# Performance work log

Hardware: AMD Instinct MI355X
Metric: run time of the kernel (lower is better)

The kernel has to match this reference:

```python
import jax, jax.numpy as jnp
import numpy as np

BETA = 0.25  # loss_beta


def setup_inputs() -> dict:
    key = jax.random.key(0)
    k1, k2 = jax.random.split(key)
    data = jax.random.normal(k1, (65536, 256), dtype=jnp.float32)       # [N, D]
    codebooks = jax.random.normal(k2, (4, 1024, 256), dtype=jnp.float32)  # [L, K, D]
    return {"data": data, "codebooks": codebooks}


def _quantize_level(r, cb):
    # r: [N, D], cb: [K, D]
    # L2 distances via ||r||^2 + ||c||^2 - 2 r @ c^T (matches torch.addmm form)
    d2 = ((r * r).sum(-1, keepdims=True)
          + (cb * cb).sum(-1)[None, :]
          - 2.0 * (r @ cb.T))                      # [N, K]
    ids = jnp.argmin(d2, axis=-1)                  # [N]
    q = cb[ids]                                    # nearest-code gather, [N, D]
    return q, ids


def reference(data, codebooks):
    sg = jax.lax.stop_gradient
    r = data
    z_q = jnp.zeros_like(data)
    loss = jnp.zeros((), dtype=data.dtype)
    zq_list, id_list = [], []
    for i in range(codebooks.shape[0]):  # small fixed number of codebook levels
        r_in = r
        q, ids = _quantize_level(r_in, codebooks[i])
        q_st = r_in + sg(q - r_in)                 # straight-through estimator
        z_q = z_q + q_st
        # commitment + codebook loss (standard RQ-VAE)
        loss = loss + BETA * jnp.mean((sg(q) - r_in) ** 2) \
                    + jnp.mean((q - sg(r_in)) ** 2)
        r = r_in - q                               # residual for next level
        zq_list.append(z_q)
        id_list.append(ids)
    zq_stack = jnp.stack(zq_list)                  # [L, N, D] accumulated quantizations
    semantic_ids = jnp.stack(id_list, axis=-1)     # [N, L]
    return zq_stack, semantic_ids, loss
```

## Files before the change

kernel.cpp:

```cpp
#include <hip/hip_runtime.h>
#include <hip/hip_bf16.h>


#define NROWS   65536
#define DIM     256
#define KCODES  1024
#define LEVELS  4
#define CH      (NROWS * DIM)
#define IDS_OFF (LEVELS * CH)

#define BM      256
#define NCHUNK  8
#define CAP     32
#define MARGIN  8.0f
#define CHUNK_USH 32768
#define LVL_USH 262144

typedef __attribute__((ext_vector_type(8))) short bf16x8;
typedef __attribute__((ext_vector_type(4))) float f32x4;
typedef const __attribute__((address_space(1))) void* gp_t;
typedef __attribute__((address_space(3))) void* lp_t;

__device__ __forceinline__ unsigned short f2bf(float x) {
    __hip_bfloat16 h = __float2bfloat16(x);
    unsigned short r; __builtin_memcpy(&r, &h, 2); return r;
}
__device__ __forceinline__ float bf2f(unsigned short u) {
    __hip_bfloat16 h; __builtin_memcpy(&h, &u, 2); return __bfloat162float(h);
}

__global__ __launch_bounds__(64) void k_prep(const float* __restrict__ cb,
                                             unsigned short* __restrict__ cbw,
                                             float* __restrict__ cn2w,
                                             double* __restrict__ cn2d) {
    int cr = blockIdx.x;
    int L = cr >> 10, c = cr & 1023;
    int l = threadIdx.x;
    float4 v = *(const float4*)(cb + (size_t)cr * DIM + l * 4);
    ushort4 st;
    st.x = f2bf(v.x); st.y = f2bf(v.y); st.z = f2bf(v.z); st.w = f2bf(v.w);
    int b = l * 8;
    int kk = b >> 6, g = (b >> 4) & 3, h = (b & 15) >> 1;
    int idx = ((((L * 16 + (c >> 6)) * 4 + ((c >> 4) & 3)) * 8 + kk) * 64
               + (g * 16 + (c & 15))) * 8 + h;
    *(ushort4*)(cbw + idx) = st;
    float f0 = bf2f(st.x), f1 = bf2f(st.y), f2 = bf2f(st.z), f3 = bf2f(st.w);
    float sq = f0 * f0 + f1 * f1 + f2 * f2 + f3 * f3;
    double dq = (double)v.x * v.x + (double)v.y * v.y
              + (double)v.z * v.z + (double)v.w * v.w;
    #pragma unroll
    for (int m = 32; m; m >>= 1) {
        sq += __shfl_xor(sq, m);
        dq += __shfl_xor(dq, m);
    }
    if (l == 0) { cn2w[cr] = sq; cn2d[cr] = dq; }
}

__global__ __launch_bounds__(1024) void k_score(
    const float* rsrc,
    const float* __restrict__ cbf,
    const unsigned short* __restrict__ cbwL,
    const float* __restrict__ cn2L,
    const double* __restrict__ cn2dL,
    int* __restrict__ wid_out,
    float* rnext,
    int level)
{
    __shared__ unsigned short cbuf[2 * CHUNK_USH];
    __shared__ unsigned short cand[BM * CAP];
    __shared__ int cnt[BM];
    __shared__ int winid[BM];

    const int tid = threadIdx.x;
    const int w = tid >> 6, l = tid & 63;
    const int g = l >> 4, li = l & 15;
    const int rows0 = blockIdx.x * BM;

    #define STAGE(T) do {                                                      \
        const unsigned short* _g = cbwL + (T) * CHUNK_USH;                     \
        unsigned short* _d = &cbuf[((T) & 1) * CHUNK_USH];                     \
        _Pragma("unroll")                                                      \
        for (int _r = 0; _r < 4; ++_r)                                         \
            __builtin_amdgcn_global_load_lds((gp_t)(_g + _r * 8192 + tid * 8), \
                                             (lp_t)(_d + _r * 8192 + tid * 8), \
                                             16, 0, 0);                        \
    } while (0)

    STAGE(0);
    if (tid < BM) cnt[tid] = 0;

    bf16x8 af[8];
    {
        int row = rows0 + w * 16 + li;
        const float* rp = rsrc + (size_t)row * DIM;
        #pragma unroll
        for (int kk = 0; kk < 8; ++kk) {
            int d0 = kk * 32 + 8 * g;
            float4 v0 = *(const float4*)(rp + d0);
            float4 v1 = *(const float4*)(rp + d0 + 4);
            bf16x8 t;
            t[0] = (short)f2bf(v0.x); t[1] = (short)f2bf(v0.y);
            t[2] = (short)f2bf(v0.z); t[3] = (short)f2bf(v0.w);
            t[4] = (short)f2bf(v1.x); t[5] = (short)f2bf(v1.y);
            t[6] = (short)f2bf(v1.z); t[7] = (short)f2bf(v1.w);
            af[kk] = t;
        }
    }

    float minv[4];
    float sbuf[8][4];
    #pragma unroll
    for (int rg = 0; rg < 4; ++rg) minv[rg] = 3.0e38f;

    __syncthreads();

    for (int kc = 0; kc < NCHUNK; ++kc) {
        if (kc < NCHUNK - 1) STAGE(kc + 1);
        const unsigned short* fb = &cbuf[(kc & 1) * CHUNK_USH];

        #pragma unroll
        for (int nt = 0; nt < 8; ++nt) {
            f32x4 acc = {0.f, 0.f, 0.f, 0.f};
            const unsigned short* fp8 = fb + (nt * 8) * 512 + l * 8;
            #pragma unroll
            for (int kk = 0; kk < 8; ++kk) {
                bf16x8 bfr = *(const bf16x8*)(fp8 + kk * 512);
                acc = __builtin_amdgcn_mfma_f32_16x16x32_bf16(af[kk], bfr, acc, 0, 0, 0);
            }
            float c2 = cn2L[kc * 128 + nt * 16 + li];
            #pragma unroll
            for (int rg = 0; rg < 4; ++rg) {
                float v = __builtin_fmaf(-2.f, acc[rg], c2);
                sbuf[nt][rg] = v;
                minv[rg] = fminf(minv[rg], v);
            }
        }

        float rowm[4];
        #pragma unroll
        for (int rg = 0; rg < 4; ++rg) {
            float v = minv[rg];
            v = fminf(v, __shfl_xor(v, 1));
            v = fminf(v, __shfl_xor(v, 2));
            v = fminf(v, __shfl_xor(v, 4));
            v = fminf(v, __shfl_xor(v, 8));
            minv[rg] = v;
            rowm[rg] = v + MARGIN;
        }

        #pragma unroll
        for (int nt = 0; nt < 8; ++nt) {
            bool any = false;
            #pragma unroll
            for (int rg = 0; rg < 4; ++rg)
                any |= (sbuf[nt][rg] < rowm[rg]);
            if (__any(any)) {
                #pragma unroll
                for (int rg = 0; rg < 4; ++rg)
                    if (sbuf[nt][rg] < rowm[rg]) {
                        int row = w * 16 + 4 * g + rg;
                        int slot = atomicAdd(&cnt[row], 1);
                        if (slot < CAP)
                            cand[row * CAP + slot] =
                                (unsigned short)(kc * 128 + nt * 16 + li);
                    }
            }
        }
        __syncthreads();
    }

    {
        const int gg = l >> 4;
        const int q4 = l & 15;
        for (int rr = 0; rr < 16; ++rr) {
            int row = w * 16 + rr;
            int k = cnt[row];
            if (k == 1) {
                if (l == 0) winid[row] = (int)cand[row * CAP];
                continue;
            }
            bool list = (k >= 1 && k <= CAP);
            int total = list ? k : KCODES;
            int grow = rows0 + row;
            const float* rrow = rsrc + (size_t)grow * DIM;
            float4 rv[4];
            #pragma unroll
            for (int j = 0; j < 4; ++j)
                rv[j] = *(const float4*)(rrow + q4 * 4 + j * 64);
            double bestS = 1.0e300; int bestI = 0x7fffffff;
            for (int base = 0; base < total; base += 4) {
                int slot = base + gg;
                bool valid = slot < total;
                int code = valid ? (list ? (int)cand[row * CAP + slot] : slot) : 0;
                const float* crow = cbf + (size_t)code * DIM;
                double acc = 0.0;
                #pragma unroll
                for (int j = 0; j < 4; ++j) {
                    float4 cv = *(const float4*)(crow + q4 * 4 + j * 64);
                    acc = fma((double)cv.x, (double)rv[j].x, acc);
                    acc = fma((double)cv.y, (double)rv[j].y, acc);
                    acc = fma((double)cv.z, (double)rv[j].z, acc);
                    acc = fma((double)cv.w, (double)rv[j].w, acc);
                }
                #pragma unroll
                for (int m = 1; m <= 8; m <<= 1) acc += __shfl_xor(acc, m);
                double s = valid ? (cn2dL[code] - 2.0 * acc) : 1.0e300;
                #pragma unroll
                for (int gq = 0; gq < 4; ++gq) {
                    double sg = __shfl(s, gq * 16);
                    int cg = __shfl(code, gq * 16);
                    if ((base + gq) < total &&
                        (sg < bestS || (sg == bestS && cg < bestI))) {
                        bestS = sg; bestI = cg;
                    }
                }
            }
            if (l == 0) winid[row] = bestI;
        }
    }
    __syncthreads();

    if (tid < BM)
        wid_out[(size_t)(rows0 + tid) * LEVELS + level] = winid[tid];
    if (rnext) {
        #pragma unroll
        for (int it = 0; it < 16; ++it) {
            int rowloc = it * 16 + w;
            int grow = rows0 + rowloc;
            int d0 = l * 4;
            int code = winid[rowloc];
            float4 q = *(const float4*)(cbf + (size_t)code * DIM + d0);
            float4 r = *(const float4*)(rsrc + (size_t)grow * DIM + d0);
            float4 rn;
            rn.x = r.x - q.x; rn.y = r.y - q.y;
            rn.z = r.z - q.z; rn.w = r.w - q.w;
            *(float4*)(rnext + (size_t)grow * DIM + d0) = rn;
        }
    }
}

__global__ __launch_bounds__(256) void k_final(
    const float* __restrict__ data,
    const float* __restrict__ cbf0,
    int* wid,
    float* __restrict__ zq,
    double* __restrict__ blockpart)
{
    __shared__ float wl[4];
    const int tid = threadIdx.x;
    const int w = tid >> 6, l = tid & 63;
    const int rows0 = blockIdx.x * 32;
    float lacc = 0.f;
    #pragma unroll
    for (int i = 0; i < 8; ++i) {
        int grow = rows0 + i * 4 + w;
        int4 c4 = *(const int4*)(wid + (size_t)grow * LEVELS);
        int d0 = l * 4;
        float4 r = *(const float4*)(data + (size_t)grow * DIM + d0);
        float4 z = {0.f, 0.f, 0.f, 0.f};
        int codes[4] = {c4.x, c4.y, c4.z, c4.w};
        #pragma unroll
        for (int lv = 0; lv < LEVELS; ++lv) {
            const float* crow = cbf0 + ((size_t)lv * KCODES + codes[lv]) * DIM;
            float4 q = *(const float4*)(crow + d0);
            float dx = q.x - r.x, dy = q.y - r.y, dz = q.z - r.z, dw = q.w - r.w;
            z.x += (r.x + dx); z.y += (r.y + dy);
            z.z += (r.z + dz); z.w += (r.w + dw);
            *(float4*)(zq + (size_t)lv * CH + (size_t)grow * DIM + d0) = z;
            lacc += dx * dx + dy * dy + dz * dz + dw * dw;
            r.x = -dx; r.y = -dy; r.z = -dz; r.w = -dw;
        }
        if (l == 0) {
            float4 f; f.x = (float)codes[0]; f.y = (float)codes[1];
            f.z = (float)codes[2]; f.w = (float)codes[3];
            *(float4*)((float*)wid + (size_t)grow * LEVELS) = f;
        }
    }
    #pragma unroll
    for (int m = 32; m; m >>= 1) lacc += __shfl_xor(lacc, m);
    if (l == 0) wl[w] = lacc;
    __syncthreads();
    if (tid == 0)
        blockpart[blockIdx.x] =
            (double)wl[0] + (double)wl[1] + (double)wl[2] + (double)wl[3];
}

__global__ __launch_bounds__(256) void k_loss(const double* __restrict__ part,
                                              float* __restrict__ loss) {
    __shared__ double sd[256];
    int tid = threadIdx.x;
    double a = 0.0;
    #pragma unroll
    for (int i = 0; i < 8; ++i) a += part[i * 256 + tid];
    sd[tid] = a; __syncthreads();
    for (int s = 128; s > 0; s >>= 1) {
        if (tid < s) sd[tid] += sd[tid + s];
        __syncthreads();
    }
    if (tid == 0) *loss = (float)(sd[0] * (1.25 / 16777216.0));
}

extern "C" void kernel_launch(void* const* d_in, const int* in_sizes, int n_in,
                              void* d_out, int out_size, void* d_ws, size_t ws_size,
                              hipStream_t stream) {
    const float* data = (const float*)d_in[0];
    const float* cb   = (const float*)d_in[1];
    float* out  = (float*)d_out;
    float* zq   = out;
    int*   wid  = (int*)(out + IDS_OFF);
    float* loss = out + IDS_OFF + NROWS * LEVELS;
    char* ws = (char*)d_ws;
    unsigned short* cbw = (unsigned short*)ws;
    float*  cn2w  = (float*)(ws + (size_t)LEVELS * LVL_USH * 2);
    double* cn2d  = (double*)(ws + (size_t)LEVELS * LVL_USH * 2 + 16384);
    double* bpart = (double*)(ws + (size_t)LEVELS * LVL_USH * 2 + 16384 + 32768);
    float* rscr = zq + (size_t)3 * CH;

    k_prep<<<LEVELS * KCODES, 64, 0, stream>>>(cb, cbw, cn2w, cn2d);
    for (int lv = 0; lv < LEVELS; ++lv) {
        const float* rsrc = (lv == 0) ? data : rscr;
        float* rnext = (lv < 3) ? rscr : nullptr;
        k_score<<<NROWS / BM, 1024, 0, stream>>>(
            rsrc, cb + (size_t)lv * KCODES * DIM, cbw + (size_t)lv * LVL_USH,
            cn2w + (size_t)lv * KCODES, cn2d + (size_t)lv * KCODES,
            wid, rnext, lv);
    }
    k_final<<<NROWS / 32, 256, 0, stream>>>(data, cb, wid, zq, bpart);
    k_loss<<<1, 256, 0, stream>>>(bpart, loss);
}
```

Baseline: 482.0 us.

## Fuse four per-level scoring launches into one persistent kernel with cross-level prefetch

Merges the four per-level k_score launches into a single k_score4 kernel in which each block loops over all codebook levels for its own 256 rows. This is possible because the residual rows a block needs are the ones it wrote itself. The first chunk of the next level's codebook is prefetched into LDS while the current level's refinement runs, which removes launch gaps and tail drain between levels. Each level still re-reads the residual through global memory, which is now reached through __restrict__ pointers with only a block-level fence. That aliasing and the write-then-read ordering carry some correctness risk.

```diff
diff --git a/kernel.cpp b/kernel.cpp
--- a/kernel.cpp
+++ b/kernel.cpp
@@ -56,15 +56,14 @@
     if (l == 0) { cn2w[cr] = sq; cn2d[cr] = dq; }
 }
 
-__global__ __launch_bounds__(1024) void k_score(
-    const float* rsrc,
-    const float* __restrict__ cbf,
-    const unsigned short* __restrict__ cbwL,
-    const float* __restrict__ cn2L,
-    const double* __restrict__ cn2dL,
+__global__ __launch_bounds__(1024) void k_score4(
+    const float* __restrict__ data,
+    const float* __restrict__ cbf0,
+    const unsigned short* __restrict__ cbw0,
+    const float* __restrict__ cn2w,
+    const double* __restrict__ cn2d,
     int* __restrict__ wid_out,
-    float* rnext,
-    int level)
+    float* __restrict__ rscr)
 {
     __shared__ unsigned short cbuf[2 * CHUNK_USH];
     __shared__ unsigned short cand[BM * CAP];
@@ -76,8 +75,8 @@
     const int g = l >> 4, li = l & 15;
     const int rows0 = blockIdx.x * BM;
 
-    #define STAGE(T) do {                                                      \
-        const unsigned short* _g = cbwL + (T) * CHUNK_USH;                     \
+    #define STAGE(B, T) do {                                                   \
+        const unsigned short* _g = (B) + (T) * CHUNK_USH;                      \
         unsigned short* _d = &cbuf[((T) & 1) * CHUNK_USH];                     \
         _Pragma("unroll")                                                      \
         for (int _r = 0; _r < 4; ++_r)                                         \
@@ -86,156 +85,170 @@
                                              16, 0, 0);                        \
     } while (0)
 
-    STAGE(0);
-    if (tid < BM) cnt[tid] = 0;
-
-    bf16x8 af[8];
-    {
-        int row = rows0 + w * 16 + li;
-        const float* rp = rsrc + (size_t)row * DIM;
+    STAGE(cbw0, 0);
+
+    for (int lv = 0; lv < LEVELS; ++lv) {
+        const float* rsrc = lv ? (const float*)rscr : data;
+        const float* cbf  = cbf0 + (size_t)lv * KCODES * DIM;
+        const unsigned short* cbwL = cbw0 + (size_t)lv * LVL_USH;
+        const float*  cn2L  = cn2w + (size_t)lv * KCODES;
+        const double* cn2dL = cn2d + (size_t)lv * KCODES;
+        float* rnext = (lv < 3) ? rscr : nullptr;
+
+        if (tid < BM) cnt[tid] = 0;
+
+        bf16x8 af[8];
+        {
+            int row = rows0 + w * 16 + li;
+            const float* rp = rsrc + (size_t)row * DIM;
+            #pragma unroll
+            for (int kk = 0; kk < 8; ++kk) {
+                int d0 = kk * 32 + 8 * g;
+                float4 v0 = *(const float4*)(rp + d0);
+                float4 v1 = *(const float4*)(rp + d0 + 4);
+                bf16x8 t;
+                t[0] = (short)f2bf(v0.x); t[1] = (short)f2bf(v0.y);
+                t[2] = (short)f2bf(v0.z); t[3] = (short)f2bf(v0.w);
+                t[4] = (short)f2bf(v1.x); t[5] = (short)f2bf(v1.y);
+                t[6] = (short)f2bf(v1.z); t[7] = (short)f2bf(v1.w);
+                af[kk] = t;
+            }
+        }
+
+        float minv[4];
+        float sbuf[8][4];
         #pragma unroll
-        for (int kk = 0; kk < 8; ++kk) {
-            int d0 = kk * 32 + 8 * g;
-            float4 v0 = *(const float4*)(rp + d0);
-            float4 v1 = *(const float4*)(rp + d0 + 4);
-            bf16x8 t;
-            t[0] = (short)f2bf(v0.x); t[1] = (short)f2bf(v0.y);
-            t[2] = (short)f2bf(v0.z); t[3] = (short)f2bf(v0.w);
-            t[4] = (short)f2bf(v1.x); t[5] = (short)f2bf(v1.y);
-            t[6] = (short)f2bf(v1.z); t[7] = (short)f2bf(v1.w);
-            af[kk] = t;
-        }
-    }
-
-    float minv[4];
-    float sbuf[8][4];
-    #pragma unroll
-    for (int rg = 0; rg < 4; ++rg) minv[rg] = 3.0e38f;
-
-    __syncthreads();
-
-    for (int kc = 0; kc < NCHUNK; ++kc) {
-        if (kc < NCHUNK - 1) STAGE(kc + 1);
-        const unsigned short* fb = &cbuf[(kc & 1) * CHUNK_USH];
-
-        #pragma unroll
-        for (int nt = 0; nt < 8; ++nt) {
-            f32x4 acc = {0.f, 0.f, 0.f, 0.f};
-            const unsigned short* fp8 = fb + (nt * 8) * 512 + l * 8;
-            #pragma unroll
-            for (int kk = 0; kk < 8; ++kk) {
-                bf16x8 bfr = *(const bf16x8*)(fp8 + kk * 512);
-                acc = __builtin_amdgcn_mfma_f32_16x16x32_bf16(af[kk], bfr, acc, 0, 0, 0);
-            }
-            float c2 = cn2L[kc * 128 + nt * 16 + li];
+        for (int rg = 0; rg < 4; ++rg) minv[rg] = 3.0e38f;
+
+        __syncthreads();
+
+        for (int kc = 0; kc < NCHUNK; ++kc) {
+            if (kc < NCHUNK - 1) STAGE(cbwL, kc + 1);
+            const unsigned short* fb = &cbuf[(kc & 1) * CHUNK_USH];
+
+            #pragma unroll
+            for (int nt = 0; nt < 8; ++nt) {
+                f32x4 acc = {0.f, 0.f, 0.f, 0.f};
+                const unsigned short* fp8 = fb + (nt * 8) * 512 + l * 8;
+                #pragma unroll
+                for (int kk = 0; kk < 8; ++kk) {
+                    bf16x8 bfr = *(const bf16x8*)(fp8 + kk * 512);
+                    acc = __builtin_amdgcn_mfma_f32_16x16x32_bf16(af[kk], bfr, acc, 0, 0, 0);
+                }
+                float c2 = cn2L[kc * 128 + nt * 16 + li];
+                #pragma unroll
+                for (int rg = 0; rg < 4; ++rg) {
+                    float v = __builtin_fmaf(-2.f, acc[rg], c2);
+                    sbuf[nt][rg] = v;
+                    minv[rg] = fminf(minv[rg], v);
+                }
+            }
+
+            float rowm[4];
             #pragma unroll
             for (int rg = 0; rg < 4; ++rg) {
-                float v = __builtin_fmaf(-2.f, acc[rg], c2);
-                sbuf[nt][rg] = v;
-                minv[rg] = fminf(minv[rg], v);
-            }
-        }
-
-        float rowm[4];
-        #pragma unroll
-        for (int rg = 0; rg < 4; ++rg) {
-            float v = minv[rg];
-            v = fminf(v, __shfl_xor(v, 1));
-            v = fminf(v, __shfl_xor(v, 2));
-            v = fminf(v, __shfl_xor(v, 4));
-            v = fminf(v, __shfl_xor(v, 8));
-            minv[rg] = v;
-            rowm[rg] = v + MARGIN;
-        }
-
-        #pragma unroll
-        for (int nt = 0; nt < 8; ++nt) {
-            bool any = false;
-            #pragma unroll
-            for (int rg = 0; rg < 4; ++rg)
-                any |= (sbuf[nt][rg] < rowm[rg]);
-            if (__any(any)) {
+                float v = minv[rg];
+                v = fminf(v, __shfl_xor(v, 1));
+                v = fminf(v, __shfl_xor(v, 2));
+                v = fminf(v, __shfl_xor(v, 4));
+                v = fminf(v, __shfl_xor(v, 8));
+                minv[rg] = v;
+                rowm[rg] = v + MARGIN;
+            }
+
+            #pragma unroll
+            for (int nt = 0; nt < 8; ++nt) {
+                bool any = false;
                 #pragma unroll
                 for (int rg = 0; rg < 4; ++rg)
-                    if (sbuf[nt][rg] < rowm[rg]) {
-                        int row = w * 16 + 4 * g + rg;
-                        int slot = atomicAdd(&cnt[row], 1);
-                        if (slot < CAP)
-                            cand[row * CAP + slot] =
-                                (unsigned short)(kc * 128 + nt * 16 + li);
+                    any |= (sbuf[nt][rg] < rowm[rg]);
+                if (__any(any)) {
+                    #pragma unroll
+                    for (int rg = 0; rg < 4; ++rg)
+                        if (sbuf[nt][rg] < rowm[rg]) {
+                            int row = w * 16 + 4 * g + rg;
+                            int slot = atomicAdd(&cnt[row], 1);
+                            if (slot < CAP)
+                                cand[row * CAP + slot] =
+                                    (unsigned short)(kc * 128 + nt * 16 + li);
+                        }
+                }
+            }
+            __syncthreads();
+        }
+
+        if (lv < 3) STAGE(cbwL + LVL_USH, 0);
+
+        {
+            const int gg = l >> 4;
+            const int q4 = l & 15;
+            for (int rr = 0; rr < 16; ++rr) {
+                int row = w * 16 + rr;
+                int k = cnt[row];
+                if (k == 1) {
+                    if (l == 0) winid[row] = (int)cand[row * CAP];
+                    continue;
+                }
+                bool list = (k >= 1 && k <= CAP);
+                int total = list ? k : KCODES;
+                int grow = rows0 + row;
+                const float* rrow = rsrc + (size_t)grow * DIM;
+                float4 rv[4];
+                #pragma unroll
+                for (int j = 0; j < 4; ++j)
+                    rv[j] = *(const float4*)(rrow + q4 * 4 + j * 64);
+                double bestS = 1.0e300; int bestI = 0x7fffffff;
+                for (int base = 0; base < total; base += 4) {
+                    int slot = base + gg;
+                    bool valid = slot < total;
+                    int code = valid ? (list ? (int)cand[row * CAP + slot] : slot) : 0;
+                    const float* crow = cbf + (size_t)code * DIM;
+                    double acc = 0.0;
+                    #pragma unroll
+                    for (int j = 0; j < 4; ++j) {
+                        float4 cv = *(const float4*)(crow + q4 * 4 + j * 64);
+                        acc = fma((double)cv.x, (double)rv[j].x, acc);
+                        acc = fma((double)cv.y, (double)rv[j].y, acc);
+                        acc = fma((double)cv.z, (double)rv[j].z, acc);
+                        acc = fma((double)cv.w, (double)rv[j].w, acc);
                     }
+                    #pragma unroll
+                    for (int m = 1; m <= 8; m <<= 1) acc += __shfl_xor(acc, m);
+                    double s = valid ? (cn2dL[code] - 2.0 * acc) : 1.0e300;
+                    #pragma unroll
+                    for (int gq = 0; gq < 4; ++gq) {
+                        double sg = __shfl(s, gq * 16);
+                        int cg = __shfl(code, gq * 16);
+                        if ((base + gq) < total &&
+                            (sg < bestS || (sg == bestS && cg < bestI))) {
+                            bestS = sg; bestI = cg;
+                        }
+                    }
+                }
+                if (l == 0) winid[row] = bestI;
             }
         }
         __syncthreads();
-    }
-
-    {
-        const int gg = l >> 4;
-        const int q4 = l & 15;
-        for (int rr = 0; rr < 16; ++rr) {
-            int row = w * 16 + rr;
-            int k = cnt[row];
-            if (k == 1) {
-                if (l == 0) winid[row] = (int)cand[row * CAP];
-                continue;
-            }
-            bool list = (k >= 1 && k <= CAP);
-            int total = list ? k : KCODES;
-            int grow = rows0 + row;
-            const float* rrow = rsrc + (size_t)grow * DIM;
-            float4 rv[4];
-            #pragma unroll
-            for (int j = 0; j < 4; ++j)
-                rv[j] = *(const float4*)(rrow + q4 * 4 + j * 64);
-            double bestS = 1.0e300; int bestI = 0x7fffffff;
-            for (int base = 0; base < total; base += 4) {
-                int slot = base + gg;
-                bool valid = slot < total;
-                int code = valid ? (list ? (int)cand[row * CAP + slot] : slot) : 0;
-                const float* crow = cbf + (size_t)code * DIM;
-                double acc = 0.0;
-                #pragma unroll
-                for (int j = 0; j < 4; ++j) {
-                    float4 cv = *(const float4*)(crow + q4 * 4 + j * 64);
-                    acc = fma((double)cv.x, (double)rv[j].x, acc);
-                    acc = fma((double)cv.y, (double)rv[j].y, acc);
-                    acc = fma((double)cv.z, (double)rv[j].z, acc);
-                    acc = fma((double)cv.w, (double)rv[j].w, acc);
-                }
-                #pragma unroll
-                for (int m = 1; m <= 8; m <<= 1) acc += __shfl_xor(acc, m);
-                double s = valid ? (cn2dL[code] - 2.0 * acc) : 1.0e300;
-                #pragma unroll
-                for (int gq = 0; gq < 4; ++gq) {
-                    double sg = __shfl(s, gq * 16);
-                    int cg = __shfl(code, gq * 16);
-                    if ((base + gq) < total &&
-                        (sg < bestS || (sg == bestS && cg < bestI))) {
-                        bestS = sg; bestI = cg;
-                    }
-                }
-            }
-            if (l == 0) winid[row] = bestI;
-        }
-    }
-    __syncthreads();
-
-    if (tid < BM)
-        wid_out[(size_t)(rows0 + tid) * LEVELS + level] = winid[tid];
-    if (rnext) {
-        #pragma unroll
-        for (int it = 0; it < 16; ++it) {
-            int rowloc = it * 16 + w;
-            int grow = rows0 + rowloc;
-            int d0 = l * 4;
-            int code = winid[rowloc];
-            float4 q = *(const float4*)(cbf + (size_t)code * DIM + d0);
-            float4 r = *(const float4*)(rsrc + (size_t)grow * DIM + d0);
-            float4 rn;
-            rn.x = r.x - q.x; rn.y = r.y - q.y;
-            rn.z = r.z - q.z; rn.w = r.w - q.w;
-            *(float4*)(rnext + (size_t)grow * DIM + d0) = rn;
-        }
+
+        if (tid < BM)
+            wid_out[(size_t)(rows0 + tid) * LEVELS + lv] = winid[tid];
+        if (rnext) {
+            #pragma unroll
+            for (int it = 0; it < 16; ++it) {
+                int rowloc = it * 16 + w;
+                int grow = rows0 + rowloc;
+                int d0 = l * 4;
+                int code = winid[rowloc];
+                float4 q = *(const float4*)(cbf + (size_t)code * DIM + d0);
+                float4 r = *(const float4*)(rsrc + (size_t)grow * DIM + d0);
+                float4 rn;
+                rn.x = r.x - q.x; rn.y = r.y - q.y;
+                rn.z = r.z - q.z; rn.w = r.w - q.w;
+                *(float4*)(rnext + (size_t)grow * DIM + d0) = rn;
+            }
+        }
+        __threadfence_block();
+        __syncthreads();
     }
 }
 
@@ -317,14 +330,8 @@
     float* rscr = zq + (size_t)3 * CH;
 
     k_prep<<<LEVELS * KCODES, 64, 0, stream>>>(cb, cbw, cn2w, cn2d);
-    for (int lv = 0; lv < LEVELS; ++lv) {
-        const float* rsrc = (lv == 0) ? data : rscr;
-        float* rnext = (lv < 3) ? rscr : nullptr;
-        k_score<<<NROWS / BM, 1024, 0, stream>>>(
-            rsrc, cb + (size_t)lv * KCODES * DIM, cbw + (size_t)lv * LVL_USH,
-            cn2w + (size_t)lv * KCODES, cn2d + (size_t)lv * KCODES,
-            wid, rnext, lv);
-    }
+    k_score4<<<NROWS / BM, 1024, 0, stream>>>(data, cb, cbw, cn2w, cn2d,
+                                              wid, rscr);
     k_final<<<NROWS / 32, 256, 0, stream>>>(data, cb, wid, zq, bpart);
     k_loss<<<1, 256, 0, stream>>>(bpart, loss);
 }
```

After: 535.0 us. 1.11x slower.
